# Kernel tuning notes

Hardware: AMD Instinct MI355X
Metric: run time of the kernel (lower is better)

## Reference

```python
import jax, jax.numpy as jnp
import numpy as np
import math

B, S, H = 4, 2048, 1024
EMBED_DIM = 1024


def setup_inputs() -> dict:
    key = jax.random.key(0)
    ks = jax.random.split(key, 7)
    scale = 1.0 / math.sqrt(H)
    return {
        "xs": jax.random.normal(ks[0], (B, S, H), dtype=jnp.float32),
        "WQ_w": jax.random.normal(ks[1], (EMBED_DIM, H), dtype=jnp.float32) * scale,
        "WQ_b": jax.random.normal(ks[2], (EMBED_DIM,), dtype=jnp.float32) * scale,
        "WK_w": jax.random.normal(ks[3], (EMBED_DIM, H), dtype=jnp.float32) * scale,
        "WK_b": jax.random.normal(ks[4], (EMBED_DIM,), dtype=jnp.float32) * scale,
        "WV_w": jax.random.normal(ks[5], (EMBED_DIM, H), dtype=jnp.float32) * scale,
        "WV_b": jax.random.normal(ks[6], (EMBED_DIM,), dtype=jnp.float32) * scale,
    }


def reference(xs, WQ_w, WQ_b, WK_w, WK_b, WV_w, WV_b):
    # Linear projections (torch nn.Linear: x @ W.T + b)
    q = jnp.einsum('bsh,eh->bse', xs, WQ_w) + WQ_b  # [B,S,E]
    k = jnp.einsum('bsh,eh->bse', xs, WK_w) + WK_b
    v = jnp.einsum('bsh,eh->bse', xs, WV_w) + WV_b
    seq_len = xs.shape[1]
    inv_sqrt_e = 1.0 / math.sqrt(EMBED_DIM)
    qk = jnp.einsum('bqe,bke->bqk', q, k) * inv_sqrt_e  # [B,S,S]
    # causal mask: positions k > q get -inf (triu, diagonal=1)
    causal = jnp.tril(jnp.ones((seq_len, seq_len), dtype=bool))
    qk = jnp.where(causal[None, :, :], qk, -jnp.inf)
    attn = jax.nn.softmax(qk, axis=2)
    y = jnp.einsum('bqk,bke->bqe', attn, v)  # [B,S,E]
    return y
```

## Files before the change

kernel.cpp:

```cpp
#include <hip/hip_runtime.h>
#include <cstdint>
#include <cstddef>

typedef _Float16 f16;
typedef __attribute__((ext_vector_type(4))) _Float16 f16x4;
typedef __attribute__((ext_vector_type(8))) _Float16 f16x8;
typedef __attribute__((ext_vector_type(4))) float f32x4;

static constexpr int BB = 4;
static constexpr int SS = 2048;
static constexpr int EE = 1024;

static constexpr int BM = 128, BN = 128;

__device__ __forceinline__ void gload_lds16(const f16* g, f16* l) {
  __builtin_amdgcn_global_load_lds(
      (const __attribute__((address_space(1))) void*)g,
      (__attribute__((address_space(3))) void*)l, 16, 0, 0);
}

struct Frag {
  int lane, wave, wy, wx, l16, quad, quadx;
  __device__ Frag() {
    const int tid = threadIdx.x;
    lane = tid & 63; wave = tid >> 6;
    wy = wave >> 1; wx = wave & 1;
    l16 = lane & 15; quad = lane >> 4;
    quadx = quad ^ ((l16 >> 2) & 3);
  }
};

struct Stager {
  const f16* g[2];
  int l[2];
  __device__ void init(const f16* base, int ld, const Frag& fr) {
#pragma unroll
    for (int i = 0; i < 2; ++i) {
      const int c = fr.wave * 128 + i * 64 + fr.lane;
      const int row = c >> 2;
      const int kcs = (c & 3) ^ ((c >> 4) & 3);
      g[i] = base + (size_t)row * ld + kcs * 8;
      l[i] = c * 8;
    }
  }
  __device__ __forceinline__ void stage(int ko, f16* lds) const {
    gload_lds16(g[0] + ko, lds + l[0]);
    gload_lds16(g[1] + ko, lds + l[1]);
  }
};

__device__ __forceinline__ void mfma_round(
    const f16* __restrict__ Ash, const f16* __restrict__ Bsh,
    f32x4 acc[4][4], const Frag& fr)
{
  f16x8 af[4], bf[4];
#pragma unroll
  for (int mi = 0; mi < 4; ++mi)
    af[mi] = *(const f16x8*)(Ash + (fr.wy * 64 + mi * 16 + fr.l16) * 32 + fr.quadx * 8);
#pragma unroll
  for (int ni = 0; ni < 4; ++ni)
    bf[ni] = *(const f16x8*)(Bsh + (fr.wx * 64 + ni * 16 + fr.l16) * 32 + fr.quadx * 8);
#pragma unroll
  for (int mi = 0; mi < 4; ++mi)
#pragma unroll
    for (int ni = 0; ni < 4; ++ni)
      acc[mi][ni] = __builtin_amdgcn_mfma_f32_16x16x32_f16(af[mi], bf[ni], acc[mi][ni], 0, 0, 0);
}

__device__ __forceinline__ void gemm_core(
    const f16* __restrict__ A, const f16* __restrict__ Bt,
    int lda, int ldb, int kOuter,
    f16* __restrict__ Ash, f16* __restrict__ Bsh,
    f32x4 acc[4][4], const Frag& fr)
{
  Stager sa, sb;
  sa.init(A, lda, fr);
  sb.init(Bt, ldb, fr);
  for (int kt = 0; kt < kOuter; ++kt) {
    const int ko = kt * 64;
    sa.stage(ko, Ash);       sa.stage(ko + 32, Ash + 128 * 32);
    sb.stage(ko, Bsh);       sb.stage(ko + 32, Bsh + 128 * 32);
    __syncthreads();
    mfma_round(Ash, Bsh, acc, fr);
    mfma_round(Ash + 128 * 32, Bsh + 128 * 32, acc, fr);
    __syncthreads();
  }
}

__global__ __launch_bounds__(256) void cast_all_kernel(
    const float* __restrict__ xs,
    const float* __restrict__ w0, const float* __restrict__ w1, const float* __restrict__ w2,
    f16* __restrict__ Xh, f16* __restrict__ o0, f16* __restrict__ o1, f16* __restrict__ o2)
{
  const int i = blockIdx.x * 256 + threadIdx.x;
  const float* src; f16* dst; int idx;
  if (i < 2097152) {
    src = xs; dst = Xh; idx = i;
  } else {
    const int j = i - 2097152;
    const int w = j >> 18;
    idx = j & 262143;
    src = (w == 0) ? w0 : (w == 1) ? w1 : w2;
    dst = (w == 0) ? o0 : (w == 1) ? o1 : o2;
  }
  const float4 f = ((const float4*)src)[idx];
  f16x4 h;
  h.x = (f16)f.x; h.y = (f16)f.y; h.z = (f16)f.z; h.w = (f16)f.w;
  ((f16x4*)dst)[idx] = h;
}

__global__ __launch_bounds__(256, 2) void proj_kernel(
    const f16* __restrict__ X,
    const f16* __restrict__ Wq, const f16* __restrict__ Wk, const f16* __restrict__ Wv,
    const float* __restrict__ bq, const float* __restrict__ bk, const float* __restrict__ bv,
    f16* __restrict__ Qh, f16* __restrict__ Kh, f16* __restrict__ Vt)
{
  __shared__ __align__(16) f16 smem[3][2][BM * 32];
  Frag fr;
  const int t = blockIdx.x;
  if (t < 512) {
    const int row0 = (t & 63) * BM, col0 = (t >> 6) * BN;
    Stager sa, sw0, sw1;
    sa.init(X + (size_t)row0 * EE, EE, fr);
    sw0.init(Wq + (size_t)col0 * EE, EE, fr);
    sw1.init(Wk + (size_t)col0 * EE, EE, fr);

    f32x4 acc[2][4][4] = {};

    for (int kt = 0; kt < EE / 64; ++kt) {
      const int ko = kt * 64;
      sa.stage(ko, smem[0][0]);   sa.stage(ko + 32, smem[0][1]);
      sw0.stage(ko, smem[1][0]);  sw0.stage(ko + 32, smem[1][1]);
      sw1.stage(ko, smem[2][0]);  sw1.stage(ko + 32, smem[2][1]);
      __syncthreads();
#pragma unroll
      for (int h = 0; h < 2; ++h) {
        f16x8 af[4];
#pragma unroll
        for (int mi = 0; mi < 4; ++mi)
          af[mi] = *(const f16x8*)(smem[0][h] + (fr.wy * 64 + mi * 16 + fr.l16) * 32 + fr.quadx * 8);
#pragma unroll
        for (int z = 0; z < 2; ++z) {
          f16x8 bf[4];
#pragma unroll
          for (int ni = 0; ni < 4; ++ni)
            bf[ni] = *(const f16x8*)(smem[1 + z][h] + (fr.wx * 64 + ni * 16 + fr.l16) * 32 + fr.quadx * 8);
#pragma unroll
          for (int mi = 0; mi < 4; ++mi)
#pragma unroll
            for (int ni = 0; ni < 4; ++ni)
              acc[z][mi][ni] = __builtin_amdgcn_mfma_f32_16x16x32_f16(af[mi], bf[ni], acc[z][mi][ni], 0, 0, 0);
        }
      }
      __syncthreads();
    }

#pragma unroll
    for (int z = 0; z < 2; ++z) {
      const float* bias = (z == 0) ? bq : bk;
      f16* out = (z == 0) ? Qh : Kh;
#pragma unroll
      for (int ni = 0; ni < 4; ++ni) {
        const int c = col0 + fr.wx * 64 + ni * 16 + fr.l16;
        const float bv2 = bias[c];
#pragma unroll
        for (int mi = 0; mi < 4; ++mi) {
          const int r = row0 + fr.wy * 64 + mi * 16 + fr.quad * 4;
#pragma unroll
          for (int i = 0; i < 4; ++i)
            out[(size_t)(r + i) * EE + c] = (f16)(acc[z][mi][ni][i] + bv2);
        }
      }
    }
  } else {
    const int u = t - 512;
    const int row0 = (u & 7) * BM;
    const int sg0 = (u >> 3) * BN;
    const int b = sg0 / SS, s0 = sg0 % SS;
    f32x4 acc[4][4] = {};
    gemm_core(Wv + (size_t)row0 * EE, X + (size_t)sg0 * EE, EE, EE, EE / 64,
              smem[0][0], smem[1][0], acc, fr);
    f16* out = Vt + (size_t)b * EE * SS;
#pragma unroll
    for (int ni = 0; ni < 4; ++ni) {
      const int c = s0 + fr.wx * 64 + ni * 16 + fr.l16;
#pragma unroll
      for (int mi = 0; mi < 4; ++mi) {
        const int r = row0 + fr.wy * 64 + mi * 16 + fr.quad * 4;
#pragma unroll
        for (int i = 0; i < 4; ++i)
          out[(size_t)(r + i) * SS + c] = (f16)(acc[mi][ni][i] + bv[r + i]);
      }
    }
  }
}

__global__ __launch_bounds__(256) void scores_kernel(
    const f16* __restrict__ Q, const f16* __restrict__ Kh, f16* __restrict__ Sc)
{
  __shared__ __align__(16) f16 Ash[2][BM * 32];
  __shared__ __align__(16) f16 Bsh[2][BN * 32];
  const int t = blockIdx.x, b = blockIdx.z;
  int qt = 0;
  while ((qt + 1) * (qt + 2) / 2 <= t) ++qt;
  const int kt = t - qt * (qt + 1) / 2;
  const f16* A  = Q  + (size_t)b * SS * EE + (size_t)qt * BM * EE;
  const f16* Bp = Kh + (size_t)b * SS * EE + (size_t)kt * BN * EE;
  f16* out = Sc + (size_t)b * SS * SS;
  Frag fr;
  f32x4 acc[4][4] = {};
  gemm_core(A, Bp, EE, EE, EE / 64, Ash[0], Bsh[0], acc, fr);
  const float scale = 0.03125f;
#pragma unroll
  for (int ni = 0; ni < 4; ++ni) {
    const int c = kt * BN + fr.wx * 64 + ni * 16 + fr.l16;
#pragma unroll
    for (int mi = 0; mi < 4; ++mi) {
      const int r = qt * BM + fr.wy * 64 + mi * 16 + fr.quad * 4;
#pragma unroll
      for (int i = 0; i < 4; ++i)
        out[(size_t)(r + i) * SS + c] = (f16)(acc[mi][ni][i] * scale);
    }
  }
}

__global__ __launch_bounds__(256) void softmax_kernel(f16* __restrict__ Sc)
{
  const int q = blockIdx.x, b = blockIdx.y;
  f16* row = Sc + (size_t)b * SS * SS + (size_t)q * SS;
  const int n = q + 1;
  const int kend = ((q >> 7) + 1) << 7;
  const int tid = threadIdx.x;
  const int i0 = tid * 8;

  float v[8];
  if (i0 + 8 <= n) {
    const f16x8 h = *(const f16x8*)(row + i0);
#pragma unroll
    for (int j = 0; j < 8; ++j) v[j] = (float)h[j];
  } else {
#pragma unroll
    for (int j = 0; j < 8; ++j) {
      const int idx = i0 + j;
      v[j] = (idx < n) ? (float)row[idx] : -1e30f;
    }
  }

  float m = v[0];
#pragma unroll
  for (int j = 1; j < 8; ++j) m = fmaxf(m, v[j]);
  __shared__ float red[4];
#pragma unroll
  for (int off = 32; off > 0; off >>= 1) m = fmaxf(m, __shfl_down(m, off));
  if ((tid & 63) == 0) red[tid >> 6] = m;
  __syncthreads();
  m = fmaxf(fmaxf(red[0], red[1]), fmaxf(red[2], red[3]));

  float sum = 0.f;
#pragma unroll
  for (int j = 0; j < 8; ++j) {
    v[j] = (i0 + j < n) ? __expf(v[j] - m) : 0.f;
    sum += v[j];
  }
#pragma unroll
  for (int off = 32; off > 0; off >>= 1) sum += __shfl_down(sum, off);
  __syncthreads();
  if ((tid & 63) == 0) red[tid >> 6] = sum;
  __syncthreads();
  sum = red[0] + red[1] + red[2] + red[3];
  const float inv = 1.f / sum;

  if (i0 < kend) {
    f16x8 h;
#pragma unroll
    for (int j = 0; j < 8; ++j) h[j] = (f16)(v[j] * inv);
    *(f16x8*)(row + i0) = h;
  }
}

__global__ __launch_bounds__(256) void pv_kernel(
    const f16* __restrict__ P, const f16* __restrict__ Vt, float* __restrict__ Y)
{
  __shared__ __align__(16) f16 Ash[2][BM * 32];
  __shared__ __align__(16) f16 Bsh[2][BN * 32];
  const int t = blockIdx.x;
  const int u = t & 255;
  const int qh = u & 7, et = (u >> 3) & 7, b = u >> 6;
  const int qt = (t < 256) ? (15 - qh) : qh;
  const f16* A  = P  + (size_t)b * SS * SS + (size_t)qt * BM * SS;
  const f16* Bp = Vt + (size_t)b * EE * SS + (size_t)et * BN * SS;
  float* out = Y + (size_t)b * SS * EE;
  Frag fr;
  f32x4 acc[4][4] = {};
  gemm_core(A, Bp, SS, SS, (qt + 1) * 2, Ash[0], Bsh[0], acc, fr);
#pragma unroll
  for (int ni = 0; ni < 4; ++ni) {
    const int c = et * BN + fr.wx * 64 + ni * 16 + fr.l16;
#pragma unroll
    for (int mi = 0; mi < 4; ++mi) {
      const int r = qt * BM + fr.wy * 64 + mi * 16 + fr.quad * 4;
#pragma unroll
      for (int i = 0; i < 4; ++i)
        out[(size_t)(r + i) * EE + c] = acc[mi][ni][i];
    }
  }
}

extern "C" void kernel_launch(void* const* d_in, const int* in_sizes, int n_in,
                              void* d_out, int out_size, void* d_ws, size_t ws_size,
                              hipStream_t stream)
{
  const float* xs  = (const float*)d_in[0];
  const float* WQw = (const float*)d_in[1];
  const float* WQb = (const float*)d_in[2];
  const float* WKw = (const float*)d_in[3];
  const float* WKb = (const float*)d_in[4];
  const float* WVw = (const float*)d_in[5];
  const float* WVb = (const float*)d_in[6];

  const size_t ME = (size_t)BB * SS * EE;
  const size_t WE = (size_t)EE * EE;

  f16* Xh = (f16*)d_ws;
  f16* Wq = Xh + ME;
  f16* Wk = Wq + WE;
  f16* Wv = Wk + WE;
  f16* Qh = Wv + WE;
  f16* Kh = Qh + ME;
  f16* Vt = Kh + ME;
  f16* Sc = Vt + ME;

  cast_all_kernel<<<dim3(11264), 256, 0, stream>>>(
      xs, WQw, WKw, WVw, Xh, Wq, Wk, Wv);

  proj_kernel<<<dim3(1024), 256, 0, stream>>>(
      Xh, Wq, Wk, Wv, WQb, WKb, WVb, Qh, Kh, Vt);

  const int nTri = (SS / BM) * (SS / BM + 1) / 2;
  scores_kernel<<<dim3(nTri, 1, BB), 256, 0, stream>>>(Qh, Kh, Sc);

  softmax_kernel<<<dim3(SS, BB), 256, 0, stream>>>(Sc);

  pv_kernel<<<dim3(512), 256, 0, stream>>>(Sc, Vt, (float*)d_out);
}
```

Before: 256.0 us.

## Rewrite QKV projection as pipelined 256x128 GEMM with swizzled LDS

Replaces the projection kernel with a 512-thread, 256x128-tile GEMM that double-buffers A and B tiles in LDS. It issues global->LDS loads in small pieces interleaved between four MFMA quadrants, using explicit vmcnt/lgkmcnt waits, raw s_barrier and setprio. An XOR swizzle is meant to avoid LDS bank conflicts. Q, K and V become uniform 256 blocks each, and the fused Q+K tile sharing is dropped. The aim is to hide load latency and raise MFMA utilisation, at the cost of hand-counted wait counts that are fragile and one block per CU.

```diff
diff --git a/kernel.cpp b/kernel.cpp
--- a/kernel.cpp
+++ b/kernel.cpp
@@ -109,87 +109,188 @@
   ((f16x4*)dst)[idx] = h;
 }
 
-__global__ __launch_bounds__(256, 2) void proj_kernel(
+
+#define PBAR() asm volatile("s_barrier" ::: "memory")
+#define LGKM0() do { asm volatile("s_waitcnt lgkmcnt(0)" ::: "memory"); \
+                     __builtin_amdgcn_sched_barrier(0); } while (0)
+
+__global__ __launch_bounds__(512, 1) void proj2_kernel(
     const f16* __restrict__ X,
     const f16* __restrict__ Wq, const f16* __restrict__ Wk, const f16* __restrict__ Wv,
     const float* __restrict__ bq, const float* __restrict__ bk, const float* __restrict__ bv,
     f16* __restrict__ Qh, f16* __restrict__ Kh, f16* __restrict__ Vt)
 {
-  __shared__ __align__(16) f16 smem[3][2][BM * 32];
-  Frag fr;
+  __shared__ __align__(16) f16 smem[49152];
+  const int tid = threadIdx.x;
+  const int lane = tid & 63, wave = tid >> 6;
+  const int wy = wave >> 1, wx = wave & 1;
+  const int l16 = lane & 15, quad = lane >> 4;
+
   const int t = blockIdx.x;
-  if (t < 512) {
-    const int row0 = (t & 63) * BM, col0 = (t >> 6) * BN;
-    Stager sa, sw0, sw1;
-    sa.init(X + (size_t)row0 * EE, EE, fr);
-    sw0.init(Wq + (size_t)col0 * EE, EE, fr);
-    sw1.init(Wk + (size_t)col0 * EE, EE, fr);
-
-    f32x4 acc[2][4][4] = {};
-
-    for (int kt = 0; kt < EE / 64; ++kt) {
-      const int ko = kt * 64;
-      sa.stage(ko, smem[0][0]);   sa.stage(ko + 32, smem[0][1]);
-      sw0.stage(ko, smem[1][0]);  sw0.stage(ko + 32, smem[1][1]);
-      sw1.stage(ko, smem[2][0]);  sw1.stage(ko + 32, smem[2][1]);
-      __syncthreads();
-#pragma unroll
-      for (int h = 0; h < 2; ++h) {
-        f16x8 af[4];
-#pragma unroll
-        for (int mi = 0; mi < 4; ++mi)
-          af[mi] = *(const f16x8*)(smem[0][h] + (fr.wy * 64 + mi * 16 + fr.l16) * 32 + fr.quadx * 8);
-#pragma unroll
-        for (int z = 0; z < 2; ++z) {
-          f16x8 bf[4];
-#pragma unroll
-          for (int ni = 0; ni < 4; ++ni)
-            bf[ni] = *(const f16x8*)(smem[1 + z][h] + (fr.wx * 64 + ni * 16 + fr.l16) * 32 + fr.quadx * 8);
-#pragma unroll
-          for (int mi = 0; mi < 4; ++mi)
-#pragma unroll
-            for (int ni = 0; ni < 4; ++ni)
-              acc[z][mi][ni] = __builtin_amdgcn_mfma_f32_16x16x32_f16(af[mi], bf[ni], acc[z][mi][ni], 0, 0, 0);
-        }
+  const int which = t >> 8;
+  const int u = t & 255;
+  const f16* Abase; const f16* Bbase;
+  int mt, nt;
+  if (which < 2) {
+    mt = u >> 3; nt = u & 7;
+    Abase = X + (size_t)mt * 256 * EE;
+    Bbase = ((which == 0) ? Wq : Wk) + (size_t)nt * 128 * EE;
+  } else {
+    mt = u >> 6; nt = u & 63;
+    Abase = Wv + (size_t)mt * 256 * EE;
+    Bbase = X + (size_t)nt * 128 * EE;
+  }
+
+  const f16* gA[4]; int lA[4];
+  const f16* gB[2]; int lB[2];
+#pragma unroll
+  for (int h = 0; h < 2; ++h) {
+#pragma unroll
+    for (int j = 0; j < 2; ++j) {
+      const int slot = h * 1024 + wave * 128 + j * 64 + lane;
+      const int r = slot >> 3, cg = (slot & 7) ^ (r & 7);
+      gA[h * 2 + j] = Abase + (size_t)r * EE + cg * 8;
+      lA[h * 2 + j] = slot * 8;
+    }
+    const int slot = h * 512 + wave * 64 + lane;
+    const int r = slot >> 3, cg = (slot & 7) ^ (r & 7);
+    gB[h] = Bbase + (size_t)r * EE + cg * 8;
+    lB[h] = slot * 8;
+  }
+
+  auto stA = [&](int buf, int h, int kt) {
+    const int ko = kt * 64;
+    f16* base = smem + buf * 16384;
+    gload_lds16(gA[h * 2 + 0] + ko, base + lA[h * 2 + 0]);
+    gload_lds16(gA[h * 2 + 1] + ko, base + lA[h * 2 + 1]);
+  };
+  auto stB = [&](int buf, int h, int kt) {
+    f16* base = smem + 32768 + buf * 8192;
+    gload_lds16(gB[h] + kt * 64, base + lB[h]);
+  };
+
+  int offA[4][2], offB[4][2];
+#pragma unroll
+  for (int i = 0; i < 4; ++i)
+#pragma unroll
+    for (int ks = 0; ks < 2; ++ks) {
+      { const int row = wy * 64 + i * 16 + l16, c = ks * 4 + quad;
+        offA[i][ks] = (row * 8 + (c ^ (row & 7))) * 8; }
+      { const int row = wx * 64 + i * 16 + l16, c = ks * 4 + quad;
+        offB[i][ks] = (row * 8 + (c ^ (row & 7))) * 8; }
+    }
+
+  stA(0, 0, 0); stA(0, 1, 0); stB(0, 0, 0); stB(0, 1, 0);
+  stB(1, 0, 1); stA(1, 0, 1);
+
+  f32x4 acc[4][4] = {};
+
+  constexpr int NT = 16;
+  for (int kt = 0; kt < NT; ++kt) {
+    const int cur = kt & 1, nxt = cur ^ 1;
+    if (kt == NT - 1) asm volatile("s_waitcnt vmcnt(0)" ::: "memory");
+    else              asm volatile("s_waitcnt vmcnt(3)" ::: "memory");
+    PBAR();
+    const f16* Ac = smem + cur * 16384;
+    const f16* Bc = smem + 32768 + cur * 8192;
+    f16x8 a0[2][2], a1[2][2], b0[2][2], b1[2][2];
+
+#pragma unroll
+    for (int mi = 0; mi < 2; ++mi)
+#pragma unroll
+      for (int ks = 0; ks < 2; ++ks) a0[mi][ks] = *(const f16x8*)(Ac + offA[mi][ks]);
+#pragma unroll
+    for (int ni = 0; ni < 2; ++ni)
+#pragma unroll
+      for (int ks = 0; ks < 2; ++ks) b0[ni][ks] = *(const f16x8*)(Bc + offB[ni][ks]);
+    if (kt + 1 < NT) stA(nxt, 1, kt + 1);
+    PBAR(); LGKM0();
+    __builtin_amdgcn_s_setprio(1);
+#pragma unroll
+    for (int mi = 0; mi < 2; ++mi)
+#pragma unroll
+      for (int ni = 0; ni < 2; ++ni)
+#pragma unroll
+        for (int ks = 0; ks < 2; ++ks)
+          acc[mi][ni] = __builtin_amdgcn_mfma_f32_16x16x32_f16(a0[mi][ks], b0[ni][ks], acc[mi][ni], 0, 0, 0);
+    __builtin_amdgcn_s_setprio(0);
+    PBAR();
+
+#pragma unroll
+    for (int ni = 0; ni < 2; ++ni)
+#pragma unroll
+      for (int ks = 0; ks < 2; ++ks) b1[ni][ks] = *(const f16x8*)(Bc + offB[ni + 2][ks]);
+    if (kt + 1 < NT) stB(nxt, 1, kt + 1);
+    PBAR(); LGKM0();
+    __builtin_amdgcn_s_setprio(1);
+#pragma unroll
+    for (int mi = 0; mi < 2; ++mi)
+#pragma unroll
+      for (int ni = 0; ni < 2; ++ni)
+#pragma unroll
+        for (int ks = 0; ks < 2; ++ks)
+          acc[mi][ni + 2] = __builtin_amdgcn_mfma_f32_16x16x32_f16(a0[mi][ks], b1[ni][ks], acc[mi][ni + 2], 0, 0, 0);
+    __builtin_amdgcn_s_setprio(0);
+    PBAR();
+
+#pragma unroll
+    for (int mi = 0; mi < 2; ++mi)
+#pragma unroll
+      for (int ks = 0; ks < 2; ++ks) a1[mi][ks] = *(const f16x8*)(Ac + offA[mi + 2][ks]);
+    if (kt + 2 < NT) stB(cur, 0, kt + 2);
+    PBAR(); LGKM0();
+    __builtin_amdgcn_s_setprio(1);
+#pragma unroll
+    for (int mi = 0; mi < 2; ++mi)
+#pragma unroll
+      for (int ni = 0; ni < 2; ++ni)
+#pragma unroll
+        for (int ks = 0; ks < 2; ++ks)
+          acc[mi + 2][ni + 2] = __builtin_amdgcn_mfma_f32_16x16x32_f16(a1[mi][ks], b1[ni][ks], acc[mi + 2][ni + 2], 0, 0, 0);
+    __builtin_amdgcn_s_setprio(0);
+    PBAR();
+
+    if (kt + 2 < NT) stA(cur, 0, kt + 2);
+    __builtin_amdgcn_s_setprio(1);
+#pragma unroll
+    for (int mi = 0; mi < 2; ++mi)
+#pragma unroll
+      for (int ni = 0; ni < 2; ++ni)
+#pragma unroll
+        for (int ks = 0; ks < 2; ++ks)
+          acc[mi + 2][ni] = __builtin_amdgcn_mfma_f32_16x16x32_f16(a1[mi][ks], b0[ni][ks], acc[mi + 2][ni], 0, 0, 0);
+    __builtin_amdgcn_s_setprio(0);
+  }
+
+  const int r0 = mt * 256 + wy * 64;
+  const int c0 = nt * 128 + wx * 64;
+  if (which < 2) {
+    const float* bias = (which == 0) ? bq : bk;
+    f16* out = (which == 0) ? Qh : Kh;
+#pragma unroll
+    for (int ni = 0; ni < 4; ++ni) {
+      const int c = c0 + ni * 16 + l16;
+      const float bz = bias[c];
+#pragma unroll
+      for (int mi = 0; mi < 4; ++mi) {
+        const int r = r0 + mi * 16 + quad * 4;
+#pragma unroll
+        for (int i = 0; i < 4; ++i)
+          out[(size_t)(r + i) * EE + c] = (f16)(acc[mi][ni][i] + bz);
       }
-      __syncthreads();
-    }
-
-#pragma unroll
-    for (int z = 0; z < 2; ++z) {
-      const float* bias = (z == 0) ? bq : bk;
-      f16* out = (z == 0) ? Qh : Kh;
-#pragma unroll
-      for (int ni = 0; ni < 4; ++ni) {
-        const int c = col0 + fr.wx * 64 + ni * 16 + fr.l16;
-        const float bv2 = bias[c];
-#pragma unroll
-        for (int mi = 0; mi < 4; ++mi) {
-          const int r = row0 + fr.wy * 64 + mi * 16 + fr.quad * 4;
-#pragma unroll
-          for (int i = 0; i < 4; ++i)
-            out[(size_t)(r + i) * EE + c] = (f16)(acc[z][mi][ni][i] + bv2);
-        }
-      }
     }
   } else {
-    const int u = t - 512;
-    const int row0 = (u & 7) * BM;
-    const int sg0 = (u >> 3) * BN;
-    const int b = sg0 / SS, s0 = sg0 % SS;
-    f32x4 acc[4][4] = {};
-    gemm_core(Wv + (size_t)row0 * EE, X + (size_t)sg0 * EE, EE, EE, EE / 64,
-              smem[0][0], smem[1][0], acc, fr);
-    f16* out = Vt + (size_t)b * EE * SS;
 #pragma unroll
     for (int ni = 0; ni < 4; ++ni) {
-      const int c = s0 + fr.wx * 64 + ni * 16 + fr.l16;
+      const int cg = c0 + ni * 16 + l16;
+      const int b = cg >> 11, sc = cg & 2047;
+      f16* out = Vt + (size_t)b * EE * SS;
 #pragma unroll
       for (int mi = 0; mi < 4; ++mi) {
-        const int r = row0 + fr.wy * 64 + mi * 16 + fr.quad * 4;
+        const int r = r0 + mi * 16 + quad * 4;
 #pragma unroll
         for (int i = 0; i < 4; ++i)
-          out[(size_t)(r + i) * SS + c] = (f16)(acc[mi][ni][i] + bv[r + i]);
+          out[(size_t)(r + i) * SS + sc] = (f16)(acc[mi][ni][i] + bv[r + i]);
       }
     }
   }
@@ -333,7 +434,7 @@
   cast_all_kernel<<<dim3(11264), 256, 0, stream>>>(
       xs, WQw, WKw, WVw, Xh, Wq, Wk, Wv);
 
-  proj_kernel<<<dim3(1024), 256, 0, stream>>>(
+  proj2_kernel<<<dim3(768), 512, 0, stream>>>(
       Xh, Wq, Wk, Wv, WQb, WKb, WVb, Qh, Kh, Vt);
 
   const int nTri = (SS / BM) * (SS / BM + 1) / 2;
```

Measured after the change: 262.7 us. 2.6% more time.

## Double-buffer LDS staging in scores and PV GEMMs with prefetch

Applied to the files above, without the earlier changes.

Adds a gemm_core2 that issues the next 64-wide K slice's global-to-LDS loads into a second buffer before computing on the current one. It uses partial vmcnt waits and raw s_barrier in place of the two full __syncthreads per iteration. The goal is to hide global load latency behind MFMA work in the scores and PV kernels. LDS use per block doubles, to 64 KB, which may reduce occupancy. Correctness depends on the hardcoded vmcnt(8) matching the number of outstanding loads per stage.

```diff
diff --git a/kernel.cpp b/kernel.cpp
--- a/kernel.cpp
+++ b/kernel.cpp
@@ -87,6 +87,34 @@
   }
 }
 
+__device__ __forceinline__ void gemm_core2(
+    const f16* __restrict__ A, const f16* __restrict__ Bt,
+    int lda, int ldb, int kOuter,
+    f16* __restrict__ Ash, f16* __restrict__ Bsh,
+    f32x4 acc[4][4], const Frag& fr)
+{
+  Stager sa, sb;
+  sa.init(A, lda, fr);
+  sb.init(Bt, ldb, fr);
+  sa.stage(0, Ash);  sa.stage(32, Ash + 4096);
+  sb.stage(0, Bsh);  sb.stage(32, Bsh + 4096);
+  for (int kt = 0; kt < kOuter; ++kt) {
+    const int cur = kt & 1, nxt = cur ^ 1;
+    if (kt + 1 < kOuter) {
+      const int ko = (kt + 1) * 64;
+      sa.stage(ko, Ash + nxt * 8192);  sa.stage(ko + 32, Ash + nxt * 8192 + 4096);
+      sb.stage(ko, Bsh + nxt * 8192);  sb.stage(ko + 32, Bsh + nxt * 8192 + 4096);
+      asm volatile("s_waitcnt vmcnt(8)" ::: "memory");
+    } else {
+      asm volatile("s_waitcnt vmcnt(0)" ::: "memory");
+    }
+    __builtin_amdgcn_s_barrier();
+    mfma_round(Ash + cur * 8192,        Bsh + cur * 8192,        acc, fr);
+    mfma_round(Ash + cur * 8192 + 4096, Bsh + cur * 8192 + 4096, acc, fr);
+    __builtin_amdgcn_s_barrier();
+  }
+}
+
 __global__ __launch_bounds__(256) void cast_all_kernel(
     const float* __restrict__ xs,
     const float* __restrict__ w0, const float* __restrict__ w1, const float* __restrict__ w2,
@@ -198,8 +226,8 @@
 __global__ __launch_bounds__(256) void scores_kernel(
     const f16* __restrict__ Q, const f16* __restrict__ Kh, f16* __restrict__ Sc)
 {
-  __shared__ __align__(16) f16 Ash[2][BM * 32];
-  __shared__ __align__(16) f16 Bsh[2][BN * 32];
+  __shared__ __align__(16) f16 Ash[2][128 * 64];
+  __shared__ __align__(16) f16 Bsh[2][128 * 64];
   const int t = blockIdx.x, b = blockIdx.z;
   int qt = 0;
   while ((qt + 1) * (qt + 2) / 2 <= t) ++qt;
@@ -209,7 +237,7 @@
   f16* out = Sc + (size_t)b * SS * SS;
   Frag fr;
   f32x4 acc[4][4] = {};
-  gemm_core(A, Bp, EE, EE, EE / 64, Ash[0], Bsh[0], acc, fr);
+  gemm_core2(A, Bp, EE, EE, EE / 64, Ash[0], Bsh[0], acc, fr);
   const float scale = 0.03125f;
 #pragma unroll
   for (int ni = 0; ni < 4; ++ni) {
@@ -281,8 +309,8 @@
 __global__ __launch_bounds__(256) void pv_kernel(
     const f16* __restrict__ P, const f16* __restrict__ Vt, float* __restrict__ Y)
 {
-  __shared__ __align__(16) f16 Ash[2][BM * 32];
-  __shared__ __align__(16) f16 Bsh[2][BN * 32];
+  __shared__ __align__(16) f16 Ash[2][128 * 64];
+  __shared__ __align__(16) f16 Bsh[2][128 * 64];
   const int t = blockIdx.x;
   const int u = t & 255;
   const int qh = u & 7, et = (u >> 3) & 7, b = u >> 6;
@@ -292,7 +320,7 @@
   float* out = Y + (size_t)b * SS * EE;
   Frag fr;
   f32x4 acc[4][4] = {};
-  gemm_core(A, Bp, SS, SS, (qt + 1) * 2, Ash[0], Bsh[0], acc, fr);
+  gemm_core2(A, Bp, SS, SS, (qt + 1) * 2, Ash[0], Bsh[0], acc, fr);
 #pragma unroll
   for (int ni = 0; ni < 4; ++ni) {
     const int c = et * BN + fr.wx * 64 + ni * 16 + fr.l16;
```

New measurement: 261.0 us. About the same (+2.0%).

## Balance PV kernel work by split-K pairing of high and low query tiles

Applied to the files above, without the earlier changes.

The PV kernel used to give each block one query tile, so work was triangular and unbalanced. Now each of the 256 block pairs is load-balanced: one block does the first 17 k-steps of a high query tile, and the other finishes that tile and then does a full low query tile. Partial results for the high tile are combined with float atomicAdd into an output that the cast kernel now zeroes up front. This adds atomic traffic, extra zeroing writes and non-deterministic summation order.

```diff
diff --git a/kernel.cpp b/kernel.cpp
--- a/kernel.cpp
+++ b/kernel.cpp
@@ -67,17 +67,17 @@
       acc[mi][ni] = __builtin_amdgcn_mfma_f32_16x16x32_f16(af[mi], bf[ni], acc[mi][ni], 0, 0, 0);
 }
 
-__device__ __forceinline__ void gemm_core(
+__device__ __forceinline__ void gemm_core_k(
     const f16* __restrict__ A, const f16* __restrict__ Bt,
-    int lda, int ldb, int kOuter,
+    int lda, int ldb, int kstart, int kcount,
     f16* __restrict__ Ash, f16* __restrict__ Bsh,
     f32x4 acc[4][4], const Frag& fr)
 {
   Stager sa, sb;
   sa.init(A, lda, fr);
   sb.init(Bt, ldb, fr);
-  for (int kt = 0; kt < kOuter; ++kt) {
-    const int ko = kt * 64;
+  for (int kt = 0; kt < kcount; ++kt) {
+    const int ko = (kstart + kt) * 64;
     sa.stage(ko, Ash);       sa.stage(ko + 32, Ash + 128 * 32);
     sb.stage(ko, Bsh);       sb.stage(ko + 32, Bsh + 128 * 32);
     __syncthreads();
@@ -87,12 +87,27 @@
   }
 }
 
+__device__ __forceinline__ void gemm_core(
+    const f16* __restrict__ A, const f16* __restrict__ Bt,
+    int lda, int ldb, int kOuter,
+    f16* __restrict__ Ash, f16* __restrict__ Bsh,
+    f32x4 acc[4][4], const Frag& fr)
+{
+  gemm_core_k(A, Bt, lda, ldb, 0, kOuter, Ash, Bsh, acc, fr);
+}
+
 __global__ __launch_bounds__(256) void cast_all_kernel(
     const float* __restrict__ xs,
     const float* __restrict__ w0, const float* __restrict__ w1, const float* __restrict__ w2,
-    f16* __restrict__ Xh, f16* __restrict__ o0, f16* __restrict__ o1, f16* __restrict__ o2)
+    f16* __restrict__ Xh, f16* __restrict__ o0, f16* __restrict__ o1, f16* __restrict__ o2,
+    float* __restrict__ Y)
 {
   const int i = blockIdx.x * 256 + threadIdx.x;
+  if (i >= 2883584) {
+    const float4 z = {0.f, 0.f, 0.f, 0.f};
+    ((float4*)Y)[i - 2883584] = z;
+    return;
+  }
   const float* src; f16* dst; int idx;
   if (i < 2097152) {
     src = xs; dst = Xh; idx = i;
@@ -286,22 +301,59 @@
   const int t = blockIdx.x;
   const int u = t & 255;
   const int qh = u & 7, et = (u >> 3) & 7, b = u >> 6;
-  const int qt = (t < 256) ? (15 - qh) : qh;
-  const f16* A  = P  + (size_t)b * SS * SS + (size_t)qt * BM * SS;
+  const int seg = t >> 8;
+  const int qhi = 15 - qh;
+  const int Uhi = (qhi + 1) * 2;
+  const int Ulo = (qh + 1) * 2;
+  const f16* Pb = P + (size_t)b * SS * SS;
   const f16* Bp = Vt + (size_t)b * EE * SS + (size_t)et * BN * SS;
   float* out = Y + (size_t)b * SS * EE;
   Frag fr;
-  f32x4 acc[4][4] = {};
-  gemm_core(A, Bp, SS, SS, (qt + 1) * 2, Ash[0], Bsh[0], acc, fr);
-#pragma unroll
-  for (int ni = 0; ni < 4; ++ni) {
-    const int c = et * BN + fr.wx * 64 + ni * 16 + fr.l16;
-#pragma unroll
-    for (int mi = 0; mi < 4; ++mi) {
-      const int r = qt * BM + fr.wy * 64 + mi * 16 + fr.quad * 4;
-#pragma unroll
-      for (int i = 0; i < 4; ++i)
-        out[(size_t)(r + i) * EE + c] = acc[mi][ni][i];
+
+  if (seg == 0) {
+    f32x4 acc[4][4] = {};
+    gemm_core_k(Pb + (size_t)qhi * BM * SS, Bp, SS, SS, 0, 17, Ash[0], Bsh[0], acc, fr);
+#pragma unroll
+    for (int ni = 0; ni < 4; ++ni) {
+      const int c = et * BN + fr.wx * 64 + ni * 16 + fr.l16;
+#pragma unroll
+      for (int mi = 0; mi < 4; ++mi) {
+        const int r = qhi * BM + fr.wy * 64 + mi * 16 + fr.quad * 4;
+#pragma unroll
+        for (int i = 0; i < 4; ++i)
+          atomicAdd(&out[(size_t)(r + i) * EE + c], acc[mi][ni][i]);
+      }
+    }
+  } else {
+    {
+      f32x4 acc[4][4] = {};
+      gemm_core_k(Pb + (size_t)qhi * BM * SS, Bp, SS, SS, 17, Uhi - 17, Ash[0], Bsh[0], acc, fr);
+#pragma unroll
+      for (int ni = 0; ni < 4; ++ni) {
+        const int c = et * BN + fr.wx * 64 + ni * 16 + fr.l16;
+#pragma unroll
+        for (int mi = 0; mi < 4; ++mi) {
+          const int r = qhi * BM + fr.wy * 64 + mi * 16 + fr.quad * 4;
+#pragma unroll
+          for (int i = 0; i < 4; ++i)
+            atomicAdd(&out[(size_t)(r + i) * EE + c], acc[mi][ni][i]);
+        }
+      }
+    }
+    {
+      f32x4 acc[4][4] = {};
+      gemm_core_k(Pb + (size_t)qh * BM * SS, Bp, SS, SS, 0, Ulo, Ash[0], Bsh[0], acc, fr);
+#pragma unroll
+      for (int ni = 0; ni < 4; ++ni) {
+        const int c = et * BN + fr.wx * 64 + ni * 16 + fr.l16;
+#pragma unroll
+        for (int mi = 0; mi < 4; ++mi) {
+          const int r = qh * BM + fr.wy * 64 + mi * 16 + fr.quad * 4;
+#pragma unroll
+          for (int i = 0; i < 4; ++i)
+            out[(size_t)(r + i) * EE + c] = acc[mi][ni][i];
+        }
+      }
     }
   }
 }
@@ -330,8 +382,8 @@
   f16* Vt = Kh + ME;
   f16* Sc = Vt + ME;
 
-  cast_all_kernel<<<dim3(11264), 256, 0, stream>>>(
-      xs, WQw, WKw, WVw, Xh, Wq, Wk, Wv);
+  cast_all_kernel<<<dim3(19456), 256, 0, stream>>>(
+      xs, WQw, WKw, WVw, Xh, Wq, Wk, Wv, (float*)d_out);
 
   proj_kernel<<<dim3(1024), 256, 0, stream>>>(
       Xh, Wq, Wk, Wv, WQb, WKb, WVb, Qh, Kh, Vt);
```

Result: slower. 265.4 us (+3.7%).
